# Optimization experiments

Measured on AMD Instinct MI355X. Metric: run time of the kernel, lower is better.

## Reference

```python
import jax, jax.numpy as jnp
import numpy as np

B, S = 8, 1024
DM = 512            # d_model arg
D = 2 * DM          # actual feature width (1024)
H = 16
DK = D // H         # 64
DV = 2 * 32         # per-head value dim (2*d_v) = 64
DI = 2048           # d_inner
K = 4               # d_conv, dilation 2 -> effective 7, pad 3 each side
EPS = 1e-6


def setup_inputs() -> dict:
    key = jax.random.key(0)
    ks = jax.random.split(key, 16)
    s = lambda k, shape, fan: jax.random.normal(k, shape, jnp.float32) / np.sqrt(fan)
    return {
        "x": jax.random.normal(ks[0], (B, S, D), jnp.float32),
        "mask": jnp.ones((B, 1, 1, S), jnp.int32),
        "gamma": jnp.ones((D,), jnp.float32),
        "wq": s(ks[1], (D, H * DK), D),
        "wk": s(ks[2], (D, H * DK), D),
        "wv": s(ks[3], (D, H * DV), D),
        "wo": s(ks[4], (H * DV, D), H * DV),
        "w1": s(ks[5], (DM, DI), DM),
        "b1": jnp.zeros((DI,), jnp.float32),
        "cw": s(ks[6], (DI, 1, K), K),   # depthwise conv kernel [O, I/groups=1, K]
        "cb": jnp.zeros((DI,), jnp.float32),
        "w2": s(ks[7], (DM, DI), DM),
        "b2": jnp.zeros((DI,), jnp.float32),
        "wp": s(ks[8], (DI, D), DI),
        "bp": jnp.zeros((D,), jnp.float32),
    }


def reference(x, mask, gamma, wq, wk, wv, wo, w1, b1, cw, cb, w2, b2, wp, bp):
    # RMSNorm
    nrm = x * jax.lax.rsqrt(jnp.mean(x * x, axis=-1, keepdims=True) + EPS) * gamma
    # Multi-head attention
    q = (nrm @ wq).reshape(B, S, H, DK).transpose(0, 2, 1, 3)
    k = (nrm @ wk).reshape(B, S, H, DK).transpose(0, 2, 1, 3)
    v = (nrm @ wv).reshape(B, S, H, DV).transpose(0, 2, 1, 3)
    scores = jnp.einsum('bhqd,bhkd->bhqk', q, k) / np.sqrt(DK).astype(np.float32)
    scores = jnp.where(mask == 0, jnp.float32(-1e9), scores)
    attn = jax.nn.softmax(scores, axis=-1)
    ctx = jnp.einsum('bhqk,bhkd->bhqd', attn, v)        # [B,H,S,DV]
    ctx = ctx.transpose(0, 2, 1, 3).reshape(B, S, H * DV)
    out = ctx @ wo                                       # [B,S,D]
    # split into two halves
    f_in, s_in = out[:, :, :D // 2], out[:, :, D // 2:]
    # FirstSection: linear -> depthwise dilated conv (padding 'same')
    f = f_in @ w1 + b1                                   # [B,S,DI]
    f = f.transpose(0, 2, 1)                             # [B,DI,S]
    f = jax.lax.conv_general_dilated(
        f, cw, window_strides=(1,), padding=[(3, 3)], rhs_dilation=(2,),
        feature_group_count=DI, dimension_numbers=('NCH', 'OIH', 'NCH'))
    f = (f + cb[None, :, None]).transpose(0, 2, 1)       # [B,S,DI]
    # SecondSection: linear + relu
    sec = jax.nn.relu(s_in @ w2 + b2)                    # [B,S,DI]
    gated = f * sec
    return x + (gated @ wp + bp)
```

## Files before the change

### kernel.cpp

```cpp
#include <hip/hip_runtime.h>

typedef unsigned short u16;
typedef __bf16 bf16x8 __attribute__((ext_vector_type(8)));
typedef short  s16x8  __attribute__((ext_vector_type(8)));
typedef float  f32x4  __attribute__((ext_vector_type(4)));

#define LDSPAD 72

#define GLOAD16(gp, lp) __builtin_amdgcn_global_load_lds( \
  (__attribute__((address_space(1))) unsigned int*)(unsigned long long)(const void*)(gp), \
  (__attribute__((address_space(3))) unsigned int*)(lp), 16, 0, 0)

static __device__ __forceinline__ u16 f2bf(float f){
  union { float f; unsigned int u; } v; v.f = f;
  unsigned int r = v.u + 0x7fffu + ((v.u >> 16) & 1u);
  return (u16)(r >> 16);
}
static __device__ __forceinline__ float bf2f(u16 u){
  union { unsigned int u; float f; } v; v.u = ((unsigned int)u) << 16; return v.f;
}
static __device__ __forceinline__ unsigned fbits(float f){
  union { float f; unsigned u; } v; v.f = f; return v.u;
}

__global__ __launch_bounds__(256) void wtrans4_kernel(
    const float* __restrict__ in0, const float* __restrict__ in1,
    const float* __restrict__ in2, const float* __restrict__ in3,
    u16* __restrict__ out0, u16* __restrict__ out1,
    u16* __restrict__ out2, u16* __restrict__ out3, int K, int N){
  __shared__ float tile[32][33];
  int z = blockIdx.z;
  const float* in = (z == 0) ? in0 : (z == 1) ? in1 : (z == 2) ? in2 : in3;
  u16* out = (z == 0) ? out0 : (z == 1) ? out1 : (z == 2) ? out2 : out3;
  int n0 = blockIdx.x * 32, k0 = blockIdx.y * 32;
  int tx = threadIdx.x, ty = threadIdx.y;
  #pragma unroll
  for (int i = 0; i < 4; ++i)
    tile[ty + i*8][tx] = in[(size_t)(k0 + ty + i*8) * N + n0 + tx];
  __syncthreads();
  #pragma unroll
  for (int i = 0; i < 4; ++i)
    out[(size_t)(n0 + ty + i*8) * K + k0 + tx] = f2bf(tile[tx][ty + i*8]);
}

__global__ __launch_bounds__(256) void cwtrans_kernel(const float* __restrict__ cw,
                                                      float* __restrict__ cwT){
  int i = blockIdx.x * 256 + threadIdx.x;
  int c = i >> 2, j = i & 3;
  cwT[j * 2048 + c] = cw[i];
}

__global__ __launch_bounds__(256) void rmsnorm_kernel(const float* __restrict__ x,
                                                      const float* __restrict__ gamma,
                                                      u16* __restrict__ out){
  int row = blockIdx.x;
  const float* xr = x + (size_t)row * 1024;
  int tid = threadIdx.x;
  float4 xv = *(const float4*)(xr + tid * 4);
  float ss = xv.x*xv.x + xv.y*xv.y + xv.z*xv.z + xv.w*xv.w;
  #pragma unroll
  for (int off = 1; off < 64; off <<= 1) ss += __shfl_xor(ss, off);
  __shared__ float wsum[4];
  if ((tid & 63) == 0) wsum[tid >> 6] = ss;
  __syncthreads();
  float tot = wsum[0] + wsum[1] + wsum[2] + wsum[3];
  float r = rsqrtf(tot * (1.0f/1024.0f) + 1e-6f);
  const float4 gv = *(const float4*)(gamma + tid * 4);
  u16* o = out + (size_t)row * 1024 + tid * 4;
  o[0] = f2bf(xv.x * r * gv.x);
  o[1] = f2bf(xv.y * r * gv.y);
  o[2] = f2bf(xv.z * r * gv.z);
  o[3] = f2bf(xv.w * r * gv.w);
}

template<int EPI>
__global__ __launch_bounds__(256) void gemm128_kernel(
    const u16* __restrict__ A, int lda,
    const u16* __restrict__ Bt,
    const float* __restrict__ bias,
    const float* __restrict__ b2x,
    u16* __restrict__ outb, float* __restrict__ outf,
    u16* __restrict__ vt,
    int N, int K, float scale, int nm)
{
  __shared__ __align__(16) u16 Sh[2*128*64];
  u16* As = Sh;
  u16* Bs = Sh + 128*64;
  int tid = threadIdx.x;
  int wid = tid >> 6, lane = tid & 63;
  int fr = lane & 15, fq = lane >> 4;
  int wr = wid >> 1, wc = wid & 1;
  int l = (int)blockIdx.x;
  int m0 = (l % nm) * 128, n0 = (l / nm) * 128;
  int srow = lane >> 3;
  int csw  = (lane & 7) ^ srow;
  int c7   = fr & 7;
  f32x4 acc[4][4] = {};

  const u16* Abase = A + ((EPI == 6 && n0 >= 2048) ? 512 : 0) + (size_t)m0 * lda;
  const u16* Bbase = Bt + (size_t)n0 * K;

  auto STAGE = [&](int kt){
    int k0 = kt << 6;
    #pragma unroll
    for (int i = 0; i < 4; ++i){
      int r = i*32 + wid*8;
      GLOAD16(Abase + (size_t)(r + srow) * lda + k0 + csw*8, &As[r*64]);
      GLOAD16(Bbase + (size_t)(r + srow) * K   + k0 + csw*8, &Bs[r*64]);
    }
  };

  int nt = K >> 6;
  for (int kt = 0; kt < nt; ++kt){
    if (kt) __syncthreads();
    STAGE(kt);
    __syncthreads();
    #pragma unroll
    for (int ks = 0; ks < 2; ++ks){
      bf16x8 av[4], bv[4];
      #pragma unroll
      for (int mi = 0; mi < 4; ++mi)
        av[mi] = *(const bf16x8*)&As[(wr*64 + mi*16 + fr)*64 + (((ks*4 + fq) ^ c7) * 8)];
      #pragma unroll
      for (int ni = 0; ni < 4; ++ni)
        bv[ni] = *(const bf16x8*)&Bs[(wc*64 + ni*16 + fr)*64 + (((ks*4 + fq) ^ c7) * 8)];
      #pragma unroll
      for (int mi = 0; mi < 4; ++mi)
        #pragma unroll
        for (int ni = 0; ni < 4; ++ni)
          acc[mi][ni] = __builtin_amdgcn_mfma_f32_16x16x32_bf16(av[mi], bv[ni], acc[mi][ni], 0, 0, 0);
    }
  }

  if (EPI == 5 && n0 >= 2048){
    u16* Ct = Sh;
    #pragma unroll
    for (int p = 0; p < 2; ++p){
      __syncthreads();
      if (wc == p){
        #pragma unroll
        for (int ni = 0; ni < 4; ++ni)
          #pragma unroll
          for (int mi = 0; mi < 4; ++mi){
            int cl = ni*16 + fr;
            int rl = wr*64 + mi*16 + fq*4;
            uint2 pk;
            pk.x = (unsigned)f2bf(acc[mi][ni][0]) | ((unsigned)f2bf(acc[mi][ni][1]) << 16);
            pk.y = (unsigned)f2bf(acc[mi][ni][2]) | ((unsigned)f2bf(acc[mi][ni][3]) << 16);
            *(uint2*)&Ct[cl*136 + rl] = pk;
          }
      }
      __syncthreads();
      #pragma unroll
      for (int ci = 0; ci < 4; ++ci){
        int qq = ci*256 + tid;
        int c = qq >> 4, off = (qq & 15) * 8;
        uint4 v = *(const uint4*)&Ct[c*136 + off];
        *(uint4*)&vt[(size_t)(n0 - 2048 + p*64 + c) * 8192 + m0 + off] = v;
      }
    }
    return;
  }

  #pragma unroll
  for (int ni = 0; ni < 4; ++ni){
    int col = n0 + wc*64 + ni*16 + fr;
    bool fp = (EPI != 6) || (col < 2048);
    int cc  = (EPI == 6) ? (col & 2047) : col;
    float bvv = 0.0f;
    if (EPI == 3) bvv = bias[col];
    if (EPI == 6) bvv = fp ? bias[cc] : b2x[cc];
    float scl = (EPI == 5) ? ((col < 1024) ? scale : 1.0f) : scale;
    #pragma unroll
    for (int mi = 0; mi < 4; ++mi){
      #pragma unroll
      for (int j = 0; j < 4; ++j){
        int row = m0 + wr*64 + mi*16 + fq*4 + j;
        float vv = acc[mi][ni][j] * scl + bvv;
        size_t idx = (size_t)row * N + cc;
        if (EPI == 3)      outf[idx] = vv + b2x[idx];
        else if (EPI == 6){
          if (!fp) vv = fmaxf(vv, 0.0f);
          (fp ? outb : vt)[idx] = f2bf(vv);
        } else             outb[idx] = f2bf(vv);
      }
    }
  }
}

__global__ __launch_bounds__(256) void attn_kernel(
    const u16* __restrict__ qkv, const u16* __restrict__ Vt,
    const int* __restrict__ mask, u16* __restrict__ ctx)
{
  __shared__ __align__(16) u16 Ks[2][64*64];
  __shared__ __align__(16) u16 Vs[2][64*64];
  __shared__ __align__(16) u16 Ps[64][LDSPAD];
  int tid = threadIdx.x;
  int wid = tid >> 6, lane = tid & 63;
  int fr = lane & 15, fq = lane >> 4;
  int i = (int)blockIdx.x;
  int wg = (i & 7) * 256 + (i >> 3);
  int bh = wg >> 4;
  int q0 = (wg & 15) * 64;
  int b = bh >> 4, h = bh & 15;

  const u16* qb  = qkv + (size_t)b * 1024 * 3072 + h * 64;
  const u16* kb  = qb + 1024;
  const u16* vtb = Vt + (size_t)(h * 64) * 8192 + b * 1024;

  int lrow = lane >> 3;
  int cs   = (lane & 7) ^ lrow;
  int wbase = wid * 16;
  int c7 = fr & 7;

  bf16x8 qf[2];
  {
    const u16* qp = qb + (size_t)(q0 + wid*16 + fr) * 3072 + fq * 8;
    qf[0] = *(const bf16x8*)(qp);
    qf[1] = *(const bf16x8*)(qp + 32);
  }
  f32x4 acc[4];
  #pragma unroll
  for (int k = 0; k < 4; ++k) acc[k] = (f32x4){0.f, 0.f, 0.f, 0.f};
  float mrun = -1e30f, lsum = 0.f;

  auto STAGE = [&](int bsel, int t){
    int kv0 = t * 64;
    #pragma unroll
    for (int k = 0; k < 2; ++k){
      int r = wbase + k*8 + lrow;
      GLOAD16(kb  + (size_t)(kv0 + r) * 3072 + cs * 8, &Ks[bsel][(wbase + k*8) * 64]);
      GLOAD16(vtb + (size_t)r * 8192 + kv0 + cs * 8,   &Vs[bsel][(wbase + k*8) * 64]);
    }
  };

  STAGE(0, 0);
  __syncthreads();
  for (int t = 0; t < 16; ++t){
    int cur = t & 1;
    int kv0 = t * 64;
    if (t + 1 < 16) STAGE(cur ^ 1, t + 1);

    bf16x8 kf[2][4], vf[2][4];
    #pragma unroll
    for (int ks = 0; ks < 2; ++ks)
      #pragma unroll
      for (int nt = 0; nt < 4; ++nt){
        kf[ks][nt] = *(const bf16x8*)&Ks[cur][(nt*16 + fr)*64 + (((ks*4 + fq) ^ c7) * 8)];
        vf[ks][nt] = *(const bf16x8*)&Vs[cur][(nt*16 + fr)*64 + (((ks*4 + fq) ^ c7) * 8)];
      }
    int mv1 = mask[b * 1024 + kv0 + lane];

    f32x4 sc[4];
    #pragma unroll
    for (int nt = 0; nt < 4; ++nt) sc[nt] = (f32x4){0.f, 0.f, 0.f, 0.f};
    __builtin_amdgcn_s_setprio(1);
    #pragma unroll
    for (int ks = 0; ks < 2; ++ks)
      #pragma unroll
      for (int nt = 0; nt < 4; ++nt)
        sc[nt] = __builtin_amdgcn_mfma_f32_16x16x32_bf16(kf[ks][nt], qf[ks], sc[nt], 0, 0, 0);
    __builtin_amdgcn_s_setprio(0);

    if (!__all(mv1 != 0)){
      #pragma unroll
      for (int nt = 0; nt < 4; ++nt){
        int4 mv = *(const int4*)&mask[b * 1024 + kv0 + nt*16 + fq*4];
        int mvals[4] = {mv.x, mv.y, mv.z, mv.w};
        #pragma unroll
        for (int j = 0; j < 4; ++j)
          sc[nt][j] = mvals[j] ? sc[nt][j] : -1e9f;
      }
    }

    float m01 = fmaxf(fmaxf(sc[0][0], sc[0][1]), fmaxf(sc[0][2], sc[0][3]));
    float m11 = fmaxf(fmaxf(sc[1][0], sc[1][1]), fmaxf(sc[1][2], sc[1][3]));
    float m21 = fmaxf(fmaxf(sc[2][0], sc[2][1]), fmaxf(sc[2][2], sc[2][3]));
    float m31 = fmaxf(fmaxf(sc[3][0], sc[3][1]), fmaxf(sc[3][2], sc[3][3]));
    float pmax = fmaxf(fmaxf(m01, m11), fmaxf(m21, m31));
    pmax = fmaxf(pmax, __shfl_xor(pmax, 16));
    pmax = fmaxf(pmax, __shfl_xor(pmax, 32));
    if (!__all(pmax <= mrun + 8.0f)){
      float mnew = fmaxf(mrun, pmax);
      float corr = exp2f(mrun - mnew);
      #pragma unroll
      for (int nt = 0; nt < 4; ++nt)
        #pragma unroll
        for (int j = 0; j < 4; ++j)
          acc[nt][j] *= corr;
      lsum *= corr;
      mrun = mnew;
    }
    float p[4][4];
    float ls = 0.f;
    #pragma unroll
    for (int nt = 0; nt < 4; ++nt)
      #pragma unroll
      for (int j = 0; j < 4; ++j){
        float pv = exp2f(sc[nt][j] - mrun);
        p[nt][j] = pv;
        ls += pv;
      }
    lsum += ls;

    #pragma unroll
    for (int nt = 0; nt < 4; ++nt){
      unsigned d0 = __builtin_amdgcn_perm(fbits(p[nt][1]), fbits(p[nt][0]), 0x07060302u);
      unsigned d1 = __builtin_amdgcn_perm(fbits(p[nt][3]), fbits(p[nt][2]), 0x07060302u);
      *(unsigned*)&Ps[wid*16 + fr][nt*16 + fq*4]     = d0;
      *(unsigned*)&Ps[wid*16 + fr][nt*16 + fq*4 + 2] = d1;
    }

    __builtin_amdgcn_s_setprio(1);
    #pragma unroll
    for (int ks = 0; ks < 2; ++ks){
      bf16x8 pb = *(const bf16x8*)&Ps[wid*16 + fr][ks*32 + fq*8];
      #pragma unroll
      for (int nt = 0; nt < 4; ++nt)
        acc[nt] = __builtin_amdgcn_mfma_f32_16x16x32_bf16(vf[ks][nt], pb, acc[nt], 0, 0, 0);
    }
    __builtin_amdgcn_s_setprio(0);

    __syncthreads();
  }

  lsum += __shfl_xor(lsum, 16);
  lsum += __shfl_xor(lsum, 32);
  float invl = 1.0f / lsum;

  size_t rowbase = ((size_t)b * 1024 + q0 + wid*16 + fr) * 1024 + h * 64;
  #pragma unroll
  for (int nt = 0; nt < 4; ++nt){
    unsigned lo = (unsigned)f2bf(acc[nt][0] * invl) | ((unsigned)f2bf(acc[nt][1] * invl) << 16);
    unsigned hi = (unsigned)f2bf(acc[nt][2] * invl) | ((unsigned)f2bf(acc[nt][3] * invl) << 16);
    uint2 pk; pk.x = lo; pk.y = hi;
    *(uint2*)&ctx[rowbase + nt*16 + fq*4] = pk;
  }
}

__global__ __launch_bounds__(256) void convgate_kernel(
    const u16* __restrict__ f, const float* __restrict__ cwT,
    const float* __restrict__ cb, u16* __restrict__ sec_inout)
{
  size_t gid = (size_t)blockIdx.x * blockDim.x + threadIdx.x;
  int c0 = (int)(gid & 255) * 8;
  int t  = (int)((gid >> 8) & 1023);
  int b  = (int)(gid >> 18);
  const u16* fb = f + ((size_t)b * 1024) * 2048;

  float4 w[4][2];
  #pragma unroll
  for (int j = 0; j < 4; ++j){
    w[j][0] = *(const float4*)&cwT[j*2048 + c0];
    w[j][1] = *(const float4*)&cwT[j*2048 + c0 + 4];
  }
  float4 cb0 = *(const float4*)&cb[c0];
  float4 cb1 = *(const float4*)&cb[c0 + 4];
  float acc[8] = {cb0.x, cb0.y, cb0.z, cb0.w, cb1.x, cb1.y, cb1.z, cb1.w};

  #pragma unroll
  for (int j = 0; j < 4; ++j){
    int tt = t - 3 + 2 * j;
    if (tt >= 0 && tt < 1024){
      s16x8 fv = *(const s16x8*)(fb + (size_t)tt * 2048 + c0);
      const float* wj = (const float*)&w[j][0];
      #pragma unroll
      for (int e = 0; e < 8; ++e) acc[e] += bf2f((u16)fv[e]) * wj[e];
    }
  }
  u16* sp = sec_inout + (((size_t)b * 1024 + t) * 2048 + c0);
  s16x8 sv = *(const s16x8*)sp;
  s16x8 ov;
  #pragma unroll
  for (int e = 0; e < 8; ++e) ov[e] = (short)f2bf(acc[e] * bf2f((u16)sv[e]));
  *(s16x8*)sp = ov;
}

extern "C" void kernel_launch(void* const* d_in, const int* in_sizes, int n_in,
                              void* d_out, int out_size, void* d_ws, size_t ws_size,
                              hipStream_t stream)
{
  const float* x     = (const float*)d_in[0];
  const int*   mask  = (const int*)  d_in[1];
  const float* gamma = (const float*)d_in[2];
  const float* wq    = (const float*)d_in[3];
  const float* wk    = (const float*)d_in[4];
  const float* wv    = (const float*)d_in[5];
  const float* wo    = (const float*)d_in[6];
  const float* w1    = (const float*)d_in[7];
  const float* b1    = (const float*)d_in[8];
  const float* cw    = (const float*)d_in[9];
  const float* cb    = (const float*)d_in[10];
  const float* w2    = (const float*)d_in[11];
  const float* b2    = (const float*)d_in[12];
  const float* wp    = (const float*)d_in[13];
  const float* bp    = (const float*)d_in[14];
  float* out = (float*)d_out;

  char* p = (char*)d_ws;
  auto alloc = [&](size_t bytes){ char* r = p; p += (bytes + 255) & ~(size_t)255; return r; };
  u16*   wqkvT = (u16*)alloc((size_t)3072*1024*2);
  u16*   woT   = (u16*)alloc((size_t)1024*1024*2);
  u16*   w12T  = (u16*)alloc((size_t)4096*512*2);
  u16*   wpT   = (u16*)alloc((size_t)1024*2048*2);
  float* cwT   = (float*)alloc((size_t)4*2048*4);
  u16*   nrm   = (u16*)alloc((size_t)8192*1024*2);
  u16*   qkv   = (u16*)alloc((size_t)8192*3072*2);
  u16*   sec   = (u16*)alloc((size_t)8192*2048*2);
  u16* Vt   = sec;
  u16* ao   = qkv;
  u16* fbuf = qkv + (size_t)8192*1024;
  (void)ws_size; (void)in_sizes; (void)n_in; (void)out_size;

  const float QSCALE = 0.125f * 1.44269504088896340736f;

  dim3 tb32(32, 8);
  wtrans4_kernel<<<dim3(32, 32, 4), tb32, 0, stream>>>(
      wq, wk, wv, wo,
      wqkvT, wqkvT + (size_t)1024*1024, wqkvT + (size_t)2048*1024, woT, 1024, 1024);
  wtrans4_kernel<<<dim3(64, 16, 2), tb32, 0, stream>>>(
      w1, w2, w1, w2, w12T, w12T + (size_t)2048*512, w12T, w12T + (size_t)2048*512, 512, 2048);
  wtrans4_kernel<<<dim3(32, 64, 1), tb32, 0, stream>>>(
      wp, wp, wp, wp, wpT, wpT, wpT, wpT, 2048, 1024);
  cwtrans_kernel<<<32, 256, 0, stream>>>(cw, cwT);

  rmsnorm_kernel<<<8192, 256, 0, stream>>>(x, gamma, nrm);

  gemm128_kernel<5><<<1536, 256, 0, stream>>>(nrm, 1024, wqkvT, nullptr, nullptr, qkv, nullptr, Vt, 3072, 1024, QSCALE, 64);

  attn_kernel<<<2048, 256, 0, stream>>>(qkv, Vt, mask, nrm);

  gemm128_kernel<0><<<512, 256, 0, stream>>>(nrm, 1024, woT, nullptr, nullptr, ao, nullptr, nullptr, 1024, 1024, 1.0f, 64);

  gemm128_kernel<6><<<2048, 256, 0, stream>>>(ao, 1024, w12T, b1, b2, fbuf, nullptr, sec, 2048, 512, 1.0f, 64);

  convgate_kernel<<<8192, 256, 0, stream>>>(fbuf, cwT, cb, sec);

  gemm128_kernel<3><<<512, 256, 0, stream>>>(sec, 2048, wpT, bp, x, nullptr, out, nullptr, 1024, 2048, 1.0f, 64);
}
```

Baseline: 314.2 us.

## Double-buffer GEMM LDS tiles with prefetch depth two and hoist mask check

The 128x128 GEMM kernel now keeps two LDS buffers for A and B. It issues global-to-LDS loads two k-tiles ahead and uses explicit vmcnt/lgkmcnt waits and barriers so memory traffic overlaps the MFMA work, with MFMAs raised in priority. This doubles LDS use per block (64KB), which can lower occupancy. The attention kernel now scans the whole mask row once up front to decide whether masking is needed, replacing a per-tile mask load and vote.

```diff
diff --git a/kernel.cpp b/kernel.cpp
--- a/kernel.cpp
+++ b/kernel.cpp
@@ -83,9 +83,8 @@
     u16* __restrict__ vt,
     int N, int K, float scale, int nm)
 {
-  __shared__ __align__(16) u16 Sh[2*128*64];
-  u16* As = Sh;
-  u16* Bs = Sh + 128*64;
+  __shared__ __align__(16) u16 As[2][128*64];
+  __shared__ __align__(16) u16 Bs[2][128*64];
   int tid = threadIdx.x;
   int wid = tid >> 6, lane = tid & 63;
   int fr = lane & 15, fq = lane >> 4;
@@ -100,40 +99,55 @@
   const u16* Abase = A + ((EPI == 6 && n0 >= 2048) ? 512 : 0) + (size_t)m0 * lda;
   const u16* Bbase = Bt + (size_t)n0 * K;
 
-  auto STAGE = [&](int kt){
+  auto STAGE = [&](int bsel, int kt){
     int k0 = kt << 6;
     #pragma unroll
     for (int i = 0; i < 4; ++i){
       int r = i*32 + wid*8;
-      GLOAD16(Abase + (size_t)(r + srow) * lda + k0 + csw*8, &As[r*64]);
-      GLOAD16(Bbase + (size_t)(r + srow) * K   + k0 + csw*8, &Bs[r*64]);
+      GLOAD16(Abase + (size_t)(r + srow) * lda + k0 + csw*8, &As[bsel][r*64]);
+      GLOAD16(Bbase + (size_t)(r + srow) * K   + k0 + csw*8, &Bs[bsel][r*64]);
     }
   };
 
   int nt = K >> 6;
+  STAGE(0, 0);
+  STAGE(1, 1);
+  asm volatile("s_waitcnt vmcnt(8)" ::: "memory");
+  __builtin_amdgcn_s_barrier();
   for (int kt = 0; kt < nt; ++kt){
-    if (kt) __syncthreads();
-    STAGE(kt);
-    __syncthreads();
+    int cur = kt & 1;
+    bf16x8 av[2][4], bv[2][4];
     #pragma unroll
     for (int ks = 0; ks < 2; ++ks){
-      bf16x8 av[4], bv[4];
       #pragma unroll
       for (int mi = 0; mi < 4; ++mi)
-        av[mi] = *(const bf16x8*)&As[(wr*64 + mi*16 + fr)*64 + (((ks*4 + fq) ^ c7) * 8)];
+        av[ks][mi] = *(const bf16x8*)&As[cur][(wr*64 + mi*16 + fr)*64 + (((ks*4 + fq) ^ c7) * 8)];
       #pragma unroll
       for (int ni = 0; ni < 4; ++ni)
-        bv[ni] = *(const bf16x8*)&Bs[(wc*64 + ni*16 + fr)*64 + (((ks*4 + fq) ^ c7) * 8)];
+        bv[ks][ni] = *(const bf16x8*)&Bs[cur][(wc*64 + ni*16 + fr)*64 + (((ks*4 + fq) ^ c7) * 8)];
+    }
+    asm volatile("s_waitcnt lgkmcnt(0)" ::: "memory");
+    __builtin_amdgcn_sched_barrier(0);
+    __builtin_amdgcn_s_barrier();
+    if (kt + 2 < nt) STAGE(cur, kt + 2);
+    __builtin_amdgcn_s_setprio(1);
+    #pragma unroll
+    for (int ks = 0; ks < 2; ++ks)
       #pragma unroll
       for (int mi = 0; mi < 4; ++mi)
         #pragma unroll
         for (int ni = 0; ni < 4; ++ni)
-          acc[mi][ni] = __builtin_amdgcn_mfma_f32_16x16x32_bf16(av[mi], bv[ni], acc[mi][ni], 0, 0, 0);
+          acc[mi][ni] = __builtin_amdgcn_mfma_f32_16x16x32_bf16(av[ks][mi], bv[ks][ni], acc[mi][ni], 0, 0, 0);
+    __builtin_amdgcn_s_setprio(0);
+    if (kt + 1 < nt){
+      if (kt + 2 < nt) asm volatile("s_waitcnt vmcnt(8)" ::: "memory");
+      else             asm volatile("s_waitcnt vmcnt(0)" ::: "memory");
+      __builtin_amdgcn_s_barrier();
     }
   }
 
   if (EPI == 5 && n0 >= 2048){
-    u16* Ct = Sh;
+    u16* Ct = &As[0][0];
     #pragma unroll
     for (int p = 0; p < 2; ++p){
       __syncthreads();
@@ -213,6 +227,18 @@
   int wbase = wid * 16;
   int c7 = fr & 7;
 
+  bool needmask;
+  {
+    const int4* mrow = (const int4*)&mask[b * 1024];
+    int nz = 1;
+    #pragma unroll
+    for (int k = 0; k < 4; ++k){
+      int4 mv = mrow[lane + k*64];
+      nz &= (mv.x && mv.y && mv.z && mv.w) ? 1 : 0;
+    }
+    needmask = !__all(nz);
+  }
+
   bf16x8 qf[2];
   {
     const u16* qp = qb + (size_t)(q0 + wid*16 + fr) * 3072 + fq * 8;
@@ -249,7 +275,6 @@
         kf[ks][nt] = *(const bf16x8*)&Ks[cur][(nt*16 + fr)*64 + (((ks*4 + fq) ^ c7) * 8)];
         vf[ks][nt] = *(const bf16x8*)&Vs[cur][(nt*16 + fr)*64 + (((ks*4 + fq) ^ c7) * 8)];
       }
-    int mv1 = mask[b * 1024 + kv0 + lane];
 
     f32x4 sc[4];
     #pragma unroll
@@ -262,7 +287,7 @@
         sc[nt] = __builtin_amdgcn_mfma_f32_16x16x32_bf16(kf[ks][nt], qf[ks], sc[nt], 0, 0, 0);
     __builtin_amdgcn_s_setprio(0);
 
-    if (!__all(mv1 != 0)){
+    if (needmask){
       #pragma unroll
       for (int nt = 0; nt < 4; ++nt){
         int4 mv = *(const int4*)&mask[b * 1024 + kv0 + nt*16 + fq*4];
```

Measured after the change: 310.3 us. About the same (-1.2%).
